# Optimization experiments

Hardware: AMD Instinct MI355X
Metric: run time of the kernel (lower is better)

## Reference

```python
import jax, jax.numpy as jnp
import numpy as np

H = 200
W = 200
SH = 2.0  # h / h_meters = 200/100
SW = 2.0
THRESH = 0.05   # opacity prune threshold
CHUNK = 128     # gaussians per scan step
EPS_T = 1e-4    # 3DGS transmittance early-stop
ALPHA_MIN = 1.0 / 255.0


def _rasterize(means3D, colors, opac, cov3D):
    """Orthographic BEV 3D-Gaussian-splat rasterization for one sample.
    means3D (N,3), colors (N,d), opac (N,1), cov3D (N,6) packed [xx,xy,xz,yy,yz,zz].
    Returns (d, H, W) image. Depth is identically 0 under the BEV view matrix,
    so compositing order is the input order (stable), matching the CUDA sort.
    """
    N, d = colors.shape
    P = H * W
    # pixel centers, row-major flatten: p = y*W + x
    gy, gx = jnp.meshgrid(jnp.arange(H, dtype=jnp.float32),
                          jnp.arange(W, dtype=jnp.float32), indexing='ij')
    pxf = gx.reshape(-1)
    pyf = gy.reshape(-1)

    # project means with full_proj_transform: u = -sh*y + H/2, v = -sw*x + W/2
    u = -SH * means3D[:, 1] + H / 2.0
    v = -SW * means3D[:, 0] + W / 2.0

    # 2D covariance: W2 @ Cov3D @ W2^T + 0.3*I with W2 = [[0,sh,0],[sw,0,0]]
    a = SH * SH * cov3D[:, 3] + 0.3   # var along image x (from Sigma_yy)
    c = SW * SW * cov3D[:, 0] + 0.3   # var along image y (from Sigma_xx)
    b = SH * SW * cov3D[:, 1]
    det = a * c - b * b
    valid = det > 0.0
    det_s = jnp.where(valid, det, 1.0)
    conA = c / det_s
    conB = b / det_s   # power uses +conB*dx*dy (conic.y = -b/det in CUDA)
    conC = a / det_s

    # fold pruning mask (opacity threshold) and validity into opacity
    op = jnp.where((opac[:, 0] > THRESH) & valid, opac[:, 0], 0.0)

    K = N // CHUNK
    chunks = tuple(t.reshape(K, CHUNK, *t.shape[1:])
                   for t in (u, v, conA, conB, conC, op, colors))

    def body(carry, ch):
        img, T = carry  # img (P,d), T (P,)
        u_, v_, A_, B_, C_, op_, col_ = ch
        dx = u_[:, None] - pxf[None, :]          # (C,P)
        dy = v_[:, None] - pyf[None, :]
        power = -0.5 * (A_[:, None] * dx * dx + C_[:, None] * dy * dy) \
                + B_[:, None] * dx * dy
        alpha = jnp.minimum(0.99, op_[:, None] * jnp.exp(jnp.minimum(power, 0.0)))
        # CUDA skips power>0 and alpha < 1/255
        alpha = jnp.where((power > 0.0) | (alpha < ALPHA_MIN), 0.0, alpha)
        # early termination: skip gaussian i (and all after) once T would drop < 1e-4
        T_incl = T[None, :] * jnp.cumprod(1.0 - alpha, axis=0)
        alpha = jnp.where(T_incl < EPS_T, 0.0, alpha)
        cp = jnp.cumprod(1.0 - alpha, axis=0)    # inclusive products
        T_excl = jnp.concatenate([jnp.ones((1, P), dtype=cp.dtype), cp[:-1]], axis=0)
        wgt = alpha * T_excl * T[None, :]        # (C,P)
        img = img + jnp.einsum('cp,cd->pd', wgt, col_)
        T = T * cp[-1]
        return (img, T), None

    img0 = jnp.zeros((P, d), dtype=colors.dtype)
    T0 = jnp.ones((P,), dtype=colors.dtype)
    (img, T), _ = jax.lax.scan(body, (img0, T0), chunks)
    # background is zeros -> no bg term; reshape to (d, H, W)
    return img.reshape(H, W, d).transpose(2, 0, 1)


def setup_inputs() -> dict:
    key = jax.random.key(0)
    k1, k2, k3, k4 = jax.random.split(key, 4)
    B, N, D = 2, 1024, 32
    features = jax.random.normal(k1, (B, N, D), dtype=jnp.float32)
    # BEV covers +/-50m; scale positions so most gaussians land on the canvas
    means3D = jax.random.normal(k2, (B, N, 3), dtype=jnp.float32) * 20.0
    cov3D = jax.random.uniform(k3, (B, N, 6), dtype=jnp.float32)
    opacities = jax.random.uniform(k4, (B, N, 1), dtype=jnp.float32)
    return {"features": features, "means3D": means3D,
            "cov3D": cov3D, "opacities": opacities}


def reference(features, means3D, cov3D, opacities):
    bev = jax.vmap(_rasterize)(means3D, features, opacities, cov3D)  # (B,d,H,W)
    mask = opacities[..., 0] > THRESH
    mean_count = mask.astype(jnp.float32).sum(axis=1).mean()
    return bev, mean_count
```

## Files before the change

kernel.cpp:

```cpp
#include <hip/hip_runtime.h>


#define HH 200
#define WW 200
#define DD 32
#define NG 1024
#define BB 2
#define CHUNKG 128

__global__ __launch_bounds__(256) void render_kernel(
    const float* __restrict__ feats,
    const float* __restrict__ means,
    const float* __restrict__ cov,
    const float* __restrict__ opac,
    float* __restrict__ out)
{
    __shared__ float cu_[CHUNKG], cv_[CHUNKG], cA_[CHUNKG], cB_[CHUNKG],
                     cC_[CHUNKG], cop_[CHUNKG], cpl_[CHUNKG];
    __shared__ int   cg_[CHUNKG];
    __shared__ int   wcnt[2];

    const int b    = blockIdx.z;
    const int tid  = threadIdx.y * 16 + threadIdx.x;
    const int lane = tid & 63;
    const int wid  = tid >> 6;
    const int px   = blockIdx.x * 16 + threadIdx.x;
    const int py   = blockIdx.y * 16 + threadIdx.y;
    const float pxf = (float)px;
    const float pyf = (float)py;
    const float x0  = (float)(blockIdx.x * 16);
    const float y0  = (float)(blockIdx.y * 16);

    const float* __restrict__ featsB = feats + (size_t)b * NG * DD;
    const float* __restrict__ meansB = means + (size_t)b * NG * 3;
    const float* __restrict__ covB   = cov   + (size_t)b * NG * 6;
    const float* __restrict__ opacB  = opac  + (size_t)b * NG;

    float acc[DD];
#pragma unroll
    for (int d = 0; d < DD; ++d) acc[d] = 0.f;
    float T = 1.f;

    for (int c0 = 0; c0 < NG; c0 += CHUNKG) {
        bool flag = false;
        float u = 0.f, v = 0.f, A = 0.f, Bc = 0.f, Cc = 0.f, o = 0.f, pl = 0.f;
        const int g = c0 + tid;
        if (tid < CHUNKG) {
            o = opacB[g];
            float cxx = covB[g*6+0], cxy = covB[g*6+1], cyy = covB[g*6+3];
            float a  = 4.f*cyy + 0.3f;
            float cc = 4.f*cxx + 0.3f;
            float bb = 4.f*cxy;
            float det = a*cc - bb*bb;
            if (o > 0.05f && det > 0.f) {
                float inv = 1.f / det;
                A = cc*inv; Bc = bb*inv; Cc = a*inv;
                float mx = meansB[g*3+0], my = meansB[g*3+1];
                u = -2.f*my + 100.f;
                v = -2.f*mx + 100.f;
                pl = -__logf(255.f*o);
                float qmax = -2.f*pl;
                float htr = 0.5f*(A + Cc);
                float hdf = 0.5f*(A - Cc);
                float lmin = htr - sqrtf(hdf*hdf + Bc*Bc);
                float r = sqrtf(qmax / lmin) + 0.5f;
                flag = (u >= x0 - r) && (u <= x0 + 15.f + r) &&
                       (v >= y0 - r) && (v <= y0 + 15.f + r);
            }
        }
        unsigned long long mask = __ballot(flag);

        __syncthreads();
        if (lane == 0 && wid < 2) wcnt[wid] = (int)__popcll(mask);
        __syncthreads();
        const int m = wcnt[0] + wcnt[1];
        if (flag) {
            int pos = (wid == 1 ? wcnt[0] : 0)
                    + (int)__popcll(mask & ((1ull << lane) - 1ull));
            cu_[pos] = u;  cv_[pos] = v;  cA_[pos] = A;  cB_[pos] = Bc;
            cC_[pos] = Cc; cop_[pos] = o; cpl_[pos] = pl; cg_[pos] = g;
        }
        __syncthreads();

        float P = 1.f;
        for (int i = 0; i < m; ++i) {
            float dx = cu_[i] - pxf;
            float dy = cv_[i] - pyf;
            float pw = -0.5f*(cA_[i]*dx*dx + cC_[i]*dy*dy) + cB_[i]*dx*dy;
            if (pw > 0.f) continue;
            if (pw < cpl_[i] - 1e-3f) continue;
            float alpha = fminf(0.99f, cop_[i] * __expf(pw));
            if (alpha < (1.f/255.f)) continue;
            float om = 1.f - alpha;
            float tp = T * P;
            if (tp * om < 1e-4f) break;
            float w = alpha * tp;
            const float* col = featsB + (size_t)cg_[i] * DD;
#pragma unroll
            for (int d = 0; d < DD; ++d) acc[d] = fmaf(w, col[d], acc[d]);
            P *= om;
        }
        T *= P;
    }

    if (px < WW && py < HH) {
        size_t base = (size_t)b * DD * (HH*WW) + (size_t)py * WW + px;
#pragma unroll
        for (int d = 0; d < DD; ++d)
            out[base + (size_t)d * (HH*WW)] = acc[d];
    }
}

__global__ __launch_bounds__(256) void count_kernel(
    const float* __restrict__ opac, float* __restrict__ out)
{
    const int tid = threadIdx.x;
    float s = 0.f;
    for (int i = tid; i < BB * NG; i += 256)
        s += (opac[i] > 0.05f) ? 1.f : 0.f;
#pragma unroll
    for (int off = 32; off > 0; off >>= 1)
        s += __shfl_down(s, off, 64);
    __shared__ float ws[4];
    if ((tid & 63) == 0) ws[tid >> 6] = s;
    __syncthreads();
    if (tid == 0)
        out[(size_t)BB * DD * HH * WW] = (ws[0] + ws[1] + ws[2] + ws[3]) / (float)BB;
}

extern "C" void kernel_launch(void* const* d_in, const int* in_sizes, int n_in,
                              void* d_out, int out_size, void* d_ws, size_t ws_size,
                              hipStream_t stream) {
    const float* feats = (const float*)d_in[0];
    const float* means = (const float*)d_in[1];
    const float* cvr   = (const float*)d_in[2];
    const float* opc   = (const float*)d_in[3];
    float* out = (float*)d_out;

    dim3 grid((WW + 15) / 16, (HH + 15) / 16, BB);
    dim3 block(16, 16, 1);
    render_kernel<<<grid, block, 0, stream>>>(feats, means, cvr, opc, out);
    count_kernel<<<1, 256, 0, stream>>>(opc, out);
}
```

Before: 86.67 us.

## Precompute gaussian params in prepass and render 8x8 tiles with one wavefront

A prepass kernel computes per-gaussian projected centre, conic, log threshold and radius once into workspace and also performs the opacity count, replacing the separate count kernel. The render kernel now uses 8x8-pixel tiles with a single 64-lane wavefront, so culling is tighter and needs no cross-wave synchronisation. Feature reads use float4, and a wave-wide early exit stops when every pixel's transmittance is saturated. This adds a kernel launch and a workspace round trip, and the chunk size changes the points at which the T-stop check applies.

Result: no change. 86.54 us (-0.1%).

```diff
diff --git a/kernel.cpp b/kernel.cpp
--- a/kernel.cpp
+++ b/kernel.cpp
@@ -6,126 +6,143 @@
 #define DD 32
 #define NG 1024
 #define BB 2
-#define CHUNKG 128
+#define TOTG (BB*NG)
+#define OUT_IMG (BB*DD*HH*WW)
 
-__global__ __launch_bounds__(256) void render_kernel(
-    const float* __restrict__ feats,
+
+__global__ __launch_bounds__(256) void prepass_kernel(
     const float* __restrict__ means,
     const float* __restrict__ cov,
     const float* __restrict__ opac,
+    float* __restrict__ ws,
     float* __restrict__ out)
 {
-    __shared__ float cu_[CHUNKG], cv_[CHUNKG], cA_[CHUNKG], cB_[CHUNKG],
-                     cC_[CHUNKG], cop_[CHUNKG], cpl_[CHUNKG];
-    __shared__ int   cg_[CHUNKG];
-    __shared__ int   wcnt[2];
+    const int g = blockIdx.x * 256 + threadIdx.x;
+    if (g < TOTG) {
+        float o   = opac[g];
+        float cxx = cov[g*6+0], cxy = cov[g*6+1], cyy = cov[g*6+3];
+        float a   = 4.f*cyy + 0.3f;
+        float cc  = 4.f*cxx + 0.3f;
+        float bb  = 4.f*cxy;
+        float det = a*cc - bb*bb;
+        float u=0.f, v=0.f, A=0.f, Bc=0.f, Cc=0.f, pl=0.f, r=-1.f;
+        if (o > 0.05f && det > 0.f) {
+            float inv = 1.f/det;
+            A = cc*inv; Bc = bb*inv; Cc = a*inv;
+            float mx = means[g*3+0], my = means[g*3+1];
+            u = -2.f*my + 100.f;
+            v = -2.f*mx + 100.f;
+            pl = -__logf(255.f*o);
+            float qmax = -2.f*pl;
+            float htr = 0.5f*(A+Cc), hdf = 0.5f*(A-Cc);
+            float lmin = htr - sqrtf(hdf*hdf + Bc*Bc);
+            r = sqrtf(qmax/lmin) + 0.5f;
+        }
+        ws[0*TOTG+g]=u;  ws[1*TOTG+g]=v;  ws[2*TOTG+g]=A;  ws[3*TOTG+g]=Bc;
+        ws[4*TOTG+g]=Cc; ws[5*TOTG+g]=o;  ws[6*TOTG+g]=pl; ws[7*TOTG+g]=r;
+    }
+    if (blockIdx.x == 0) {
+        const int tid = threadIdx.x;
+        float s = 0.f;
+        for (int i = tid; i < TOTG; i += 256)
+            s += (opac[i] > 0.05f) ? 1.f : 0.f;
+#pragma unroll
+        for (int off = 32; off > 0; off >>= 1)
+            s += __shfl_down(s, off, 64);
+        __shared__ float wsum[4];
+        if ((tid & 63) == 0) wsum[tid >> 6] = s;
+        __syncthreads();
+        if (tid == 0)
+            out[OUT_IMG] = (wsum[0]+wsum[1]+wsum[2]+wsum[3]) / (float)BB;
+    }
+}
+
+__global__ __launch_bounds__(64) void render_kernel(
+    const float* __restrict__ feats,
+    const float* __restrict__ ws,
+    float* __restrict__ out)
+{
+    __shared__ float su[64], sv[64], sA[64], sB[64], sC[64], sop[64], spl[64];
+    __shared__ int   sg[64];
 
     const int b    = blockIdx.z;
-    const int tid  = threadIdx.y * 16 + threadIdx.x;
-    const int lane = tid & 63;
-    const int wid  = tid >> 6;
-    const int px   = blockIdx.x * 16 + threadIdx.x;
-    const int py   = blockIdx.y * 16 + threadIdx.y;
-    const float pxf = (float)px;
-    const float pyf = (float)py;
-    const float x0  = (float)(blockIdx.x * 16);
-    const float y0  = (float)(blockIdx.y * 16);
+    const int lane = threadIdx.x;
+    const int px   = blockIdx.x*8 + (lane & 7);
+    const int py   = blockIdx.y*8 + (lane >> 3);
+    const float pxf = (float)px, pyf = (float)py;
+    const float cx  = blockIdx.x*8 + 3.5f;
+    const float cy  = blockIdx.y*8 + 3.5f;
 
     const float* __restrict__ featsB = feats + (size_t)b * NG * DD;
-    const float* __restrict__ meansB = means + (size_t)b * NG * 3;
-    const float* __restrict__ covB   = cov   + (size_t)b * NG * 6;
-    const float* __restrict__ opacB  = opac  + (size_t)b * NG;
+    const int gbase = b * NG;
 
-    float acc[DD];
+    float4 acc[8];
 #pragma unroll
-    for (int d = 0; d < DD; ++d) acc[d] = 0.f;
-    float T = 1.f;
+    for (int j = 0; j < 8; ++j) acc[j] = make_float4(0.f,0.f,0.f,0.f);
+    float T = 1.f, P = 1.f;
+    bool skip = false;
 
-    for (int c0 = 0; c0 < NG; c0 += CHUNKG) {
-        bool flag = false;
-        float u = 0.f, v = 0.f, A = 0.f, Bc = 0.f, Cc = 0.f, o = 0.f, pl = 0.f;
-        const int g = c0 + tid;
-        if (tid < CHUNKG) {
-            o = opacB[g];
-            float cxx = covB[g*6+0], cxy = covB[g*6+1], cyy = covB[g*6+3];
-            float a  = 4.f*cyy + 0.3f;
-            float cc = 4.f*cxx + 0.3f;
-            float bb = 4.f*cxy;
-            float det = a*cc - bb*bb;
-            if (o > 0.05f && det > 0.f) {
-                float inv = 1.f / det;
-                A = cc*inv; Bc = bb*inv; Cc = a*inv;
-                float mx = meansB[g*3+0], my = meansB[g*3+1];
-                u = -2.f*my + 100.f;
-                v = -2.f*mx + 100.f;
-                pl = -__logf(255.f*o);
-                float qmax = -2.f*pl;
-                float htr = 0.5f*(A + Cc);
-                float hdf = 0.5f*(A - Cc);
-                float lmin = htr - sqrtf(hdf*hdf + Bc*Bc);
-                float r = sqrtf(qmax / lmin) + 0.5f;
-                flag = (u >= x0 - r) && (u <= x0 + 15.f + r) &&
-                       (v >= y0 - r) && (v <= y0 + 15.f + r);
-            }
-        }
-        unsigned long long mask = __ballot(flag);
-
+    for (int k = 0; k < NG/64; ++k) {
+        const int g = gbase + k*64 + lane;
+        const float u = ws[0*TOTG+g];
+        const float v = ws[1*TOTG+g];
+        const float r = ws[7*TOTG+g];
+        const bool flag = (r > 0.f) &&
+                          (fabsf(u - cx) <= 3.5f + r) &&
+                          (fabsf(v - cy) <= 3.5f + r);
+        const unsigned long long mask = __ballot(flag);
+        const int m = (int)__popcll(mask);
         __syncthreads();
-        if (lane == 0 && wid < 2) wcnt[wid] = (int)__popcll(mask);
-        __syncthreads();
-        const int m = wcnt[0] + wcnt[1];
         if (flag) {
-            int pos = (wid == 1 ? wcnt[0] : 0)
-                    + (int)__popcll(mask & ((1ull << lane) - 1ull));
-            cu_[pos] = u;  cv_[pos] = v;  cA_[pos] = A;  cB_[pos] = Bc;
-            cC_[pos] = Cc; cop_[pos] = o; cpl_[pos] = pl; cg_[pos] = g;
+            const int pos = (int)__popcll(mask & ((1ull << lane) - 1ull));
+            su[pos]=u; sv[pos]=v;
+            sA[pos]=ws[2*TOTG+g]; sB[pos]=ws[3*TOTG+g]; sC[pos]=ws[4*TOTG+g];
+            sop[pos]=ws[5*TOTG+g]; spl[pos]=ws[6*TOTG+g];
+            sg[pos]=k*64 + lane;
         }
         __syncthreads();
 
-        float P = 1.f;
-        for (int i = 0; i < m; ++i) {
-            float dx = cu_[i] - pxf;
-            float dy = cv_[i] - pyf;
-            float pw = -0.5f*(cA_[i]*dx*dx + cC_[i]*dy*dy) + cB_[i]*dx*dy;
-            if (pw > 0.f) continue;
-            if (pw < cpl_[i] - 1e-3f) continue;
-            float alpha = fminf(0.99f, cop_[i] * __expf(pw));
-            if (alpha < (1.f/255.f)) continue;
-            float om = 1.f - alpha;
-            float tp = T * P;
-            if (tp * om < 1e-4f) break;
-            float w = alpha * tp;
-            const float* col = featsB + (size_t)cg_[i] * DD;
+        if (!skip) {
+            for (int i = 0; i < m; ++i) {
+                const float dx = su[i] - pxf;
+                const float dy = sv[i] - pyf;
+                const float pw = fmaf(sB[i], dx*dy,
+                                      -0.5f*(sA[i]*dx*dx + sC[i]*dy*dy));
+                if (pw > 0.f) continue;
+                if (pw < spl[i] - 1e-3f) continue;
+                const float alpha = fminf(0.99f, sop[i] * __expf(pw));
+                if (alpha < (1.f/255.f)) continue;
+                const float om = 1.f - alpha;
+                const float tp = T * P;
+                if (tp * om < 1e-4f) { skip = true; break; }
+                const float w = alpha * tp;
+                const float4* __restrict__ col =
+                    (const float4*)(featsB + (size_t)sg[i] * DD);
 #pragma unroll
-            for (int d = 0; d < DD; ++d) acc[d] = fmaf(w, col[d], acc[d]);
-            P *= om;
+                for (int j = 0; j < 8; ++j) {
+                    const float4 c4 = col[j];
+                    acc[j].x = fmaf(w, c4.x, acc[j].x);
+                    acc[j].y = fmaf(w, c4.y, acc[j].y);
+                    acc[j].z = fmaf(w, c4.z, acc[j].z);
+                    acc[j].w = fmaf(w, c4.w, acc[j].w);
+                }
+                P *= om;
+            }
         }
-        T *= P;
+        if (k & 1) {
+            T *= P; P = 1.f; skip = false;
+            if (__ballot(T >= 1e-4f) == 0ull) break;
+        }
     }
 
-    if (px < WW && py < HH) {
-        size_t base = (size_t)b * DD * (HH*WW) + (size_t)py * WW + px;
+    const size_t base = (size_t)b * DD * (HH*WW) + (size_t)py * WW + px;
 #pragma unroll
-        for (int d = 0; d < DD; ++d)
-            out[base + (size_t)d * (HH*WW)] = acc[d];
+    for (int j = 0; j < 8; ++j) {
+        out[base + (size_t)(4*j+0)*(HH*WW)] = acc[j].x;
+        out[base + (size_t)(4*j+1)*(HH*WW)] = acc[j].y;
+        out[base + (size_t)(4*j+2)*(HH*WW)] = acc[j].z;
+        out[base + (size_t)(4*j+3)*(HH*WW)] = acc[j].w;
     }
-}
-
-__global__ __launch_bounds__(256) void count_kernel(
-    const float* __restrict__ opac, float* __restrict__ out)
-{
-    const int tid = threadIdx.x;
-    float s = 0.f;
-    for (int i = tid; i < BB * NG; i += 256)
-        s += (opac[i] > 0.05f) ? 1.f : 0.f;
-#pragma unroll
-    for (int off = 32; off > 0; off >>= 1)
-        s += __shfl_down(s, off, 64);
-    __shared__ float ws[4];
-    if ((tid & 63) == 0) ws[tid >> 6] = s;
-    __syncthreads();
-    if (tid == 0)
-        out[(size_t)BB * DD * HH * WW] = (ws[0] + ws[1] + ws[2] + ws[3]) / (float)BB;
 }
 
 extern "C" void kernel_launch(void* const* d_in, const int* in_sizes, int n_in,
@@ -136,9 +153,8 @@
     const float* cvr   = (const float*)d_in[2];
     const float* opc   = (const float*)d_in[3];
     float* out = (float*)d_out;
+    float* wsf = (float*)d_ws;
 
-    dim3 grid((WW + 15) / 16, (HH + 15) / 16, BB);
-    dim3 block(16, 16, 1);
-    render_kernel<<<grid, block, 0, stream>>>(feats, means, cvr, opc, out);
-    count_kernel<<<1, 256, 0, stream>>>(opc, out);
+    prepass_kernel<<<dim3(TOTG/256), dim3(256), 0, stream>>>(means, cvr, opc, wsf, out);
+    render_kernel<<<dim3(WW/8, HH/8, BB), dim3(64), 0, stream>>>(feats, wsf, out);
 }
```
